# Kernel optimization log

Hardware: AMD Instinct MI355X
Metric: run time of the kernel (lower is better)

Reference implementation:

```python
import jax, jax.numpy as jnp
import numpy as np

N_NODES = 100_000
N_EDGES = 1_600_000
D_IN = 128
D_HID = 64   # hard-coded hidden width in Embedder.__init__
D_OUT = 128  # embed_dim
N_GRAPHS = 512


def setup_inputs() -> dict:
    key = jax.random.key(0)
    ks = jax.random.split(key, 10)
    x = jax.random.normal(ks[0], (N_NODES, D_IN), dtype=jnp.float32)
    edge_index = jax.random.randint(ks[1], (2, N_EDGES), 0, N_NODES, dtype=jnp.int64)
    batch_index = jnp.sort(jax.random.randint(ks[2], (N_NODES,), 0, N_GRAPHS, dtype=jnp.int64))
    def glorot(k, fan_in, fan_out):
        s = 1.0 / np.sqrt(fan_in)
        return jax.random.uniform(k, (fan_in, fan_out), jnp.float32, -s, s)
    # layer 1: SAGEConv(D_IN -> D_HID); layer 2: SAGEConv(D_HID -> D_OUT)
    return {
        "x": x,
        "W1_l": glorot(ks[3], D_IN, D_HID),   # applied to mean-aggregated neighbors
        "W1_r": glorot(ks[4], D_IN, D_HID),   # applied to root node
        "b1": jnp.zeros((D_HID,), jnp.float32),
        "W2_l": glorot(ks[5], D_HID, D_OUT),
        "W2_r": glorot(ks[6], D_HID, D_OUT),
        "b2": jnp.zeros((D_OUT,), jnp.float32),
        "edge_index": edge_index,
        "batch_index": batch_index,
    }


def _sage_conv(x, edge_index, W_l, W_r, b):
    # PyG SAGEConv with mean aggregation:
    # out_i = (mean_{j in N(i)} x_j) @ W_l + x_i @ W_r + b
    src, dst = edge_index[0], edge_index[1]
    n = x.shape[0]
    agg = jax.ops.segment_sum(x[src], dst, num_segments=n)          # [N, F]
    deg = jax.ops.segment_sum(jnp.ones((src.shape[0],), x.dtype), dst, num_segments=n)
    mean_nbr = agg / jnp.maximum(deg, 1.0)[:, None]
    return mean_nbr @ W_l + x @ W_r + b


def reference(x, W1_l, W1_r, b1, W2_l, W2_r, b2, edge_index, batch_index):
    h = _sage_conv(x, edge_index, W1_l, W1_r, b1)
    h = jax.nn.relu(h)
    h = _sage_conv(h, edge_index, W2_l, W2_r, b2)
    # F.dropout(p=0.5, training=False) -> identity in eval mode
    # gap: global mean pool per graph
    sums = jax.ops.segment_sum(h, batch_index, num_segments=N_GRAPHS)
    cnts = jax.ops.segment_sum(jnp.ones((h.shape[0],), h.dtype), batch_index, num_segments=N_GRAPHS)
    return sums / jnp.maximum(cnts, 1.0)[:, None]
```

## Files before the change

kernel.cpp:

```cpp
#include <hip/hip_runtime.h>

#define NN   100000
#define NE   1600000
#define DIN  128
#define DH   64
#define DOUT 128
#define NG   512

#define NB   391
#define EPB  6250
#define MSZ  (NB*256)

typedef short short8 __attribute__((ext_vector_type(8)));
typedef float floatx4 __attribute__((ext_vector_type(4)));

__device__ __forceinline__ unsigned short f2bf(float f) {
  unsigned b = __float_as_uint(f);
  b += 0x7FFF + ((b >> 16) & 1);
  return (unsigned short)(b >> 16);
}
__device__ __forceinline__ float bflo(unsigned u) {
  return __uint_as_float(u << 16);
}
__device__ __forceinline__ float bfhi(unsigned u) {
  return __uint_as_float(u & 0xFFFF0000u);
}
__device__ __forceinline__ unsigned pack2(float a, float b) {
  return (unsigned)f2bf(a) | ((unsigned)f2bf(b) << 16);
}

__global__ __launch_bounds__(256) void histA_kernel(
    const int* __restrict__ dst, int* __restrict__ cnt) {
  __shared__ int h[NB];
  for (int i = threadIdx.x; i < NB; i += 256) h[i] = 0;
  __syncthreads();
  int start = blockIdx.x * EPB, end = start + EPB;
  for (int e = start + threadIdx.x; e < end; e += 256)
    atomicAdd(&h[dst[e] >> 8], 1);
  __syncthreads();
  for (int b = threadIdx.x; b < NB; b += 256)
    cnt[b * 256 + blockIdx.x] = h[b];
}

__global__ __launch_bounds__(256) void reduce_kernel(
    const int* __restrict__ cnt, int* __restrict__ partials) {
  __shared__ int s[256];
  int i = blockIdx.x * 256 + threadIdx.x;
  s[threadIdx.x] = cnt[i];
  __syncthreads();
  for (int off = 128; off > 0; off >>= 1) {
    if (threadIdx.x < off) s[threadIdx.x] += s[threadIdx.x + off];
    __syncthreads();
  }
  if (threadIdx.x == 0) partials[blockIdx.x] = s[0];
}

__global__ __launch_bounds__(256) void scanpart_kernel(int* __restrict__ partials) {
  __shared__ int s[NB];
  for (int i = threadIdx.x; i < NB; i += 256) s[i] = partials[i];
  __syncthreads();
  if (threadIdx.x == 0) {
    int run = 0;
    for (int i = 0; i < NB; ++i) { int v = s[i]; s[i] = run; run += v; }
  }
  __syncthreads();
  for (int i = threadIdx.x; i < NB; i += 256) partials[i] = s[i];
}

__global__ __launch_bounds__(256) void scanfinal_kernel(
    const int* __restrict__ cnt, const int* __restrict__ partials,
    int* __restrict__ scanned) {
  __shared__ int s[256];
  int t = threadIdx.x;
  int i = blockIdx.x * 256 + t;
  int c = cnt[i];
  s[t] = c;
  __syncthreads();
  for (int off = 1; off < 256; off <<= 1) {
    int v = (t >= off) ? s[t - off] : 0;
    __syncthreads();
    s[t] += v;
    __syncthreads();
  }
  scanned[i] = s[t] - c + partials[blockIdx.x];
}

__global__ __launch_bounds__(256) void partA_kernel(
    const int* __restrict__ src, const int* __restrict__ dst,
    const int* __restrict__ scanned, int* __restrict__ part) {
  __shared__ int cur[NB];
  for (int i = threadIdx.x; i < NB; i += 256)
    cur[i] = scanned[i * 256 + blockIdx.x];
  __syncthreads();
  int start = blockIdx.x * EPB, end = start + EPB;
  for (int e = start + threadIdx.x; e < end; e += 256) {
    int d = dst[e], s = src[e];
    int pos = atomicAdd(&cur[d >> 8], 1);
    part[pos] = ((d & 255) << 17) | s;
  }
}

__global__ __launch_bounds__(256) void bucket_csr_kernel(
    const int* __restrict__ part, const int* __restrict__ scanned,
    int* __restrict__ row_start, int* __restrict__ eidx) {
  int b = blockIdx.x, t = threadIdx.x;
  int ebeg = scanned[b * 256];
  int eend = (b == NB - 1) ? NE : scanned[(b + 1) * 256];
  int nbase = b << 8;
  int nloc = NN - nbase; if (nloc > 256) nloc = 256;
  __shared__ int cntL[256];
  __shared__ int exclL[256];
  cntL[t] = 0;
  __syncthreads();
  for (int e = ebeg + t; e < eend; e += 256)
    atomicAdd(&cntL[part[e] >> 17], 1);
  __syncthreads();
  int c = cntL[t];
  exclL[t] = c;
  __syncthreads();
  for (int off = 1; off < 256; off <<= 1) {
    int v = (t >= off) ? exclL[t - off] : 0;
    __syncthreads();
    exclL[t] += v;
    __syncthreads();
  }
  int excl = exclL[t] - c;
  if (t < nloc) row_start[nbase + t] = ebeg + excl;
  if (b == NB - 1 && t == 0) row_start[NN] = NE;
  cntL[t] = excl;
  __syncthreads();
  for (int e = ebeg + t; e < eend; e += 256) {
    int v = part[e];
    int pos = atomicAdd(&cntL[v >> 17], 1);
    eidx[ebeg + pos] = v & 0x1FFFF;
  }
}

__global__ __launch_bounds__(256) void bounds_kernel(
    const int* __restrict__ batch, int* __restrict__ gs) {
  int g = blockIdx.x * 256 + threadIdx.x;
  if (g > NG) return;
  if (g == NG) { gs[NG] = NN; return; }
  int lo = 0, hi = NN;
  while (lo < hi) {
    int mid = (lo + hi) >> 1;
    if (batch[mid] < g) lo = mid + 1; else hi = mid;
  }
  gs[g] = lo;
}

__global__ __launch_bounds__(256) void split_w_kernel(
    const float* __restrict__ W1l, const float* __restrict__ W1r,
    short* __restrict__ wfrag) {
  int i = blockIdx.x * 256 + threadIdx.x;
  if (i >= DIN * DH) return;
  int k = i >> 6, n = i & 63;
  int kt = k >> 5, kin = k & 31;
  int lane = ((kin >> 3) << 4) | (n & 15);
  int j8 = kin & 7;
  int jt = n >> 4;
  float wl = W1l[i], wr = W1r[i];
  unsigned bl_ = __float_as_uint(wl);
  unsigned br_ = __float_as_uint(wr);
  short hl = (short)(bl_ >> 16);
  short hr = (short)(br_ >> 16);
  float rl = wl - __uint_as_float(bl_ & 0xFFFF0000u);
  float rr = wr - __uint_as_float(br_ & 0xFFFF0000u);
  short ll = (short)(__float_as_uint(rl) >> 16);
  short lr = (short)(__float_as_uint(rr) >> 16);
  int base0 = (((kt * 2 + 0) * 4 + jt) * 2) * 512 + lane * 8 + j8;
  int base1 = (((kt * 2 + 1) * 4 + jt) * 2) * 512 + lane * 8 + j8;
  wfrag[base0]       = hl;
  wfrag[base0 + 512] = ll;
  wfrag[base1]       = hr;
  wfrag[base1 + 512] = lr;
}

__global__ __launch_bounds__(256) void proj_mfma_kernel(
    const float* __restrict__ x, const short* __restrict__ wfrag,
    const float* __restrict__ b1, unsigned short* __restrict__ xlb,
    float* __restrict__ xr) {
  __shared__ short sB[32768];
  {
    const float4* wf4 = (const float4*)wfrag;
    float4* sB4 = (float4*)sB;
    for (int i = threadIdx.x; i < 4096; i += 256) sB4[i] = wf4[i];
  }
  __syncthreads();

  int wave = threadIdx.x >> 6;
  int lane = threadIdx.x & 63;
  int m = lane & 15, q = lane >> 4;
  int tpair = blockIdx.x * 4 + wave;
  int tile0 = tpair * 2, tile1 = tile0 + 1;
  if (tile0 >= 6250) return;

  int r0 = tile0 * 16 + m;
  int r1 = tile1 * 16 + m; if (r1 > NN - 1) r1 = NN - 1;
  const float4* xa = (const float4*)x + (size_t)r0 * 32 + q * 2;
  const float4* xb = (const float4*)x + (size_t)r1 * 32 + q * 2;

  floatx4 acc0[8], acc1[8];
#pragma unroll
  for (int a = 0; a < 8; ++a) {
    acc0[a] = (floatx4){0.f, 0.f, 0.f, 0.f};
    acc1[a] = (floatx4){0.f, 0.f, 0.f, 0.f};
  }

#pragma unroll
  for (int kt = 0; kt < 4; ++kt) {
    float4 p0 = xa[kt * 8];
    float4 p1 = xa[kt * 8 + 1];
    float4 p2 = xb[kt * 8];
    float4 p3 = xb[kt * 8 + 1];
    float af0[8] = {p0.x, p0.y, p0.z, p0.w, p1.x, p1.y, p1.z, p1.w};
    float af1[8] = {p2.x, p2.y, p2.z, p2.w, p3.x, p3.y, p3.z, p3.w};
    short8 ah0, al0, ah1, al1;
#pragma unroll
    for (int e = 0; e < 8; ++e) {
      unsigned b0 = __float_as_uint(af0[e]);
      ah0[e] = (short)(b0 >> 16);
      float lo0 = af0[e] - __uint_as_float(b0 & 0xFFFF0000u);
      al0[e] = (short)(__float_as_uint(lo0) >> 16);
      unsigned b1_ = __float_as_uint(af1[e]);
      ah1[e] = (short)(b1_ >> 16);
      float lo1 = af1[e] - __uint_as_float(b1_ & 0xFFFF0000u);
      al1[e] = (short)(__float_as_uint(lo1) >> 16);
    }
#pragma unroll
    for (int mat = 0; mat < 2; ++mat) {
#pragma unroll
      for (int jt = 0; jt < 4; ++jt) {
        int unit = ((kt * 2 + mat) * 4 + jt) * 2;
        short8 bh = *(const short8*)(sB + unit * 512 + lane * 8);
        short8 bl = *(const short8*)(sB + (unit + 1) * 512 + lane * 8);
        floatx4 c0 = acc0[mat * 4 + jt];
        c0 = __builtin_amdgcn_mfma_f32_16x16x32_bf16(ah0, bh, c0, 0, 0, 0);
        c0 = __builtin_amdgcn_mfma_f32_16x16x32_bf16(ah0, bl, c0, 0, 0, 0);
        c0 = __builtin_amdgcn_mfma_f32_16x16x32_bf16(al0, bh, c0, 0, 0, 0);
        acc0[mat * 4 + jt] = c0;
        floatx4 c1 = acc1[mat * 4 + jt];
        c1 = __builtin_amdgcn_mfma_f32_16x16x32_bf16(ah1, bh, c1, 0, 0, 0);
        c1 = __builtin_amdgcn_mfma_f32_16x16x32_bf16(ah1, bl, c1, 0, 0, 0);
        c1 = __builtin_amdgcn_mfma_f32_16x16x32_bf16(al1, bh, c1, 0, 0, 0);
        acc1[mat * 4 + jt] = c1;
      }
    }
  }

#pragma unroll
  for (int jt = 0; jt < 4; ++jt) {
    int j = jt * 16 + m;
    float bj = b1[j];
    floatx4 cl0 = acc0[jt], cr0 = acc0[4 + jt];
    floatx4 cl1 = acc1[jt], cr1 = acc1[4 + jt];
#pragma unroll
    for (int r = 0; r < 4; ++r) {
      int n0 = tile0 * 16 + q * 4 + r;
      xlb[(size_t)n0 * DH + j] = f2bf(cl0[r]);
      xr[(size_t)n0 * DH + j] = cr0[r] + bj;
    }
    if (tile1 < 6250) {
#pragma unroll
      for (int r = 0; r < 4; ++r) {
        int n1 = tile1 * 16 + q * 4 + r;
        xlb[(size_t)n1 * DH + j] = f2bf(cl1[r]);
        xr[(size_t)n1 * DH + j] = cr1[r] + bj;
      }
    }
  }
}

template <bool RELU_ADD>
__global__ __launch_bounds__(256) void gather_kernel(
    const uint2* __restrict__ feat2, const int* __restrict__ row_start,
    const int* __restrict__ eidx, const float4* __restrict__ xr4,
    uint2* __restrict__ out2) {
  int t = blockIdx.x * 256 + threadIdx.x;
  int node = t >> 4;
  if (node >= NN) return;
  int fl = t & 15;
  int rs = row_start[node], re = row_start[node + 1];
  float a0 = 0.f, a1 = 0.f, a2 = 0.f, a3 = 0.f;
  int k = rs;
  for (; k + 8 <= re; k += 8) {
    uint2 v[8];
#pragma unroll
    for (int u = 0; u < 8; ++u) v[u] = feat2[(size_t)eidx[k + u] * 16 + fl];
#pragma unroll
    for (int u = 0; u < 8; ++u) {
      a0 += bflo(v[u].x); a1 += bfhi(v[u].x);
      a2 += bflo(v[u].y); a3 += bfhi(v[u].y);
    }
  }
  for (; k + 2 <= re; k += 2) {
    uint2 v0 = feat2[(size_t)eidx[k] * 16 + fl];
    uint2 v1 = feat2[(size_t)eidx[k + 1] * 16 + fl];
    a0 += bflo(v0.x) + bflo(v1.x); a1 += bfhi(v0.x) + bfhi(v1.x);
    a2 += bflo(v0.y) + bflo(v1.y); a3 += bfhi(v0.y) + bfhi(v1.y);
  }
  if (k < re) {
    uint2 v = feat2[(size_t)eidx[k] * 16 + fl];
    a0 += bflo(v.x); a1 += bfhi(v.x);
    a2 += bflo(v.y); a3 += bfhi(v.y);
  }
  float inv = 1.0f / fmaxf((float)(re - rs), 1.0f);
  a0 *= inv; a1 *= inv; a2 *= inv; a3 *= inv;
  if (RELU_ADD) {
    float4 r = xr4[(size_t)node * 16 + fl];
    a0 = fmaxf(a0 + r.x, 0.f); a1 = fmaxf(a1 + r.y, 0.f);
    a2 = fmaxf(a2 + r.z, 0.f); a3 = fmaxf(a3 + r.w, 0.f);
  }
  uint2 o;
  o.x = pack2(a0, a1);
  o.y = pack2(a2, a3);
  out2[(size_t)node * 16 + fl] = o;
}

__global__ __launch_bounds__(256) void pool_kernel(
    const unsigned short* __restrict__ hb, const unsigned short* __restrict__ mb,
    const int* __restrict__ gs, float* __restrict__ hs,
    float* __restrict__ ms) {
  int g = blockIdx.x;
  int start = gs[g], end = gs[g + 1];
  int slot = threadIdx.x >> 6, j = threadIdx.x & 63;
  float sh = 0.f, sm = 0.f;
  for (int n = start + slot; n < end; n += 4) {
    sh += bflo((unsigned)hb[(size_t)n * DH + j]);
    sm += bflo((unsigned)mb[(size_t)n * DH + j]);
  }
  __shared__ float red[2][4][DH];
  red[0][slot][j] = sh;
  red[1][slot][j] = sm;
  __syncthreads();
  if (slot == 0) {
    sh = red[0][0][j] + red[0][1][j] + red[0][2][j] + red[0][3][j];
    sm = red[1][0][j] + red[1][1][j] + red[1][2][j] + red[1][3][j];
    hs[g * DH + j] = sh;
    ms[g * DH + j] = sm;
  }
}

__global__ __launch_bounds__(128) void final_kernel(
    const float* __restrict__ hs, const float* __restrict__ ms,
    const float* __restrict__ W2l, const float* __restrict__ W2r,
    const float* __restrict__ b2, const int* __restrict__ gs,
    float* __restrict__ out) {
  int g = blockIdx.x;
  int j = threadIdx.x;
  float n = (float)(gs[g + 1] - gs[g]);
  float acc = 0.f;
#pragma unroll 8
  for (int k = 0; k < DH; ++k)
    acc += ms[g * DH + k] * W2l[k * DOUT + j] + hs[g * DH + k] * W2r[k * DOUT + j];
  float inv = 1.0f / fmaxf(n, 1.0f);
  out[g * DOUT + j] = (acc + n * b2[j]) * inv;
}

extern "C" void kernel_launch(void* const* d_in, const int* in_sizes, int n_in,
                              void* d_out, int out_size, void* d_ws, size_t ws_size,
                              hipStream_t stream) {
  (void)in_sizes; (void)n_in; (void)out_size; (void)ws_size;
  const float* x   = (const float*)d_in[0];
  const float* W1l = (const float*)d_in[1];
  const float* W1r = (const float*)d_in[2];
  const float* b1  = (const float*)d_in[3];
  const float* W2l = (const float*)d_in[4];
  const float* W2r = (const float*)d_in[5];
  const float* b2  = (const float*)d_in[6];
  const int*   ei  = (const int*)d_in[7];
  const int*   batch = (const int*)d_in[8];
  const int* src = ei;
  const int* dst = ei + NE;
  float* out = (float*)d_out;

  char* ws = (char*)d_ws;
  unsigned short* xlb = (unsigned short*)(ws);
  unsigned short* hb  = (unsigned short*)(ws + 12800000);
  unsigned short* mb  = (unsigned short*)(ws + 25600000);
  int*  part      = (int*)(ws + 51200000);
  int*  cnt       = (int*)(ws + 57600000);
  int*  scanned   = (int*)(ws + 58000384);
  float* xr       = (float*)(ws + 51200000);
  int*  eidx      = (int*)(ws + 76800000);
  int*  row_start = (int*)(ws + 83200000);
  int*   gs       = (int*)(ws + 83600128);
  float* hs       = (float*)(ws + 83604224);
  float* msum     = (float*)(ws + 83735296);
  short* wfrag    = (short*)(ws + 83900032);
  int*  partials  = (int*)(ws + 84400128);

  const int gBlocks = (NN * 16) / 256;
  const int pBlocks = 782;

  split_w_kernel<<<32, 256, 0, stream>>>(W1l, W1r, wfrag);
  histA_kernel<<<256, 256, 0, stream>>>(dst, cnt);
  reduce_kernel<<<NB, 256, 0, stream>>>(cnt, partials);
  scanpart_kernel<<<1, 256, 0, stream>>>(partials);
  scanfinal_kernel<<<NB, 256, 0, stream>>>(cnt, partials, scanned);
  partA_kernel<<<256, 256, 0, stream>>>(src, dst, scanned, part);
  bucket_csr_kernel<<<NB, 256, 0, stream>>>(part, scanned, row_start, eidx);
  bounds_kernel<<<3, 256, 0, stream>>>(batch, gs);

  proj_mfma_kernel<<<pBlocks, 256, 0, stream>>>(x, wfrag, b1, xlb, xr);
  gather_kernel<true><<<gBlocks, 256, 0, stream>>>(
      (const uint2*)xlb, row_start, eidx, (const float4*)xr, (uint2*)hb);

  gather_kernel<false><<<gBlocks, 256, 0, stream>>>(
      (const uint2*)hb, row_start, eidx, nullptr, (uint2*)mb);

  pool_kernel<<<NG, 256, 0, stream>>>(hb, mb, gs, hs, msum);
  final_kernel<<<NG, 128, 0, stream>>>(hs, msum, W2l, W2r, b2, gs, out);
}
```

Measured before the change: 266.2 us.

## Widen gather loads to 16 bytes, store root projection in bf16, fuse pool and final

```diff
diff --git a/kernel.cpp b/kernel.cpp
--- a/kernel.cpp
+++ b/kernel.cpp
@@ -179,7 +179,7 @@
 __global__ __launch_bounds__(256) void proj_mfma_kernel(
     const float* __restrict__ x, const short* __restrict__ wfrag,
     const float* __restrict__ b1, unsigned short* __restrict__ xlb,
-    float* __restrict__ xr) {
+    unsigned short* __restrict__ xrb) {
   __shared__ short sB[32768];
   {
     const float4* wf4 = (const float4*)wfrag;
@@ -258,14 +258,14 @@
     for (int r = 0; r < 4; ++r) {
       int n0 = tile0 * 16 + q * 4 + r;
       xlb[(size_t)n0 * DH + j] = f2bf(cl0[r]);
-      xr[(size_t)n0 * DH + j] = cr0[r] + bj;
+      xrb[(size_t)n0 * DH + j] = f2bf(cr0[r] + bj);
     }
     if (tile1 < 6250) {
 #pragma unroll
       for (int r = 0; r < 4; ++r) {
         int n1 = tile1 * 16 + q * 4 + r;
         xlb[(size_t)n1 * DH + j] = f2bf(cl1[r]);
-        xr[(size_t)n1 * DH + j] = cr1[r] + bj;
+        xrb[(size_t)n1 * DH + j] = f2bf(cr1[r] + bj);
       }
     }
   }
@@ -273,88 +273,100 @@
 
 template <bool RELU_ADD>
 __global__ __launch_bounds__(256) void gather_kernel(
-    const uint2* __restrict__ feat2, const int* __restrict__ row_start,
-    const int* __restrict__ eidx, const float4* __restrict__ xr4,
-    uint2* __restrict__ out2) {
+    const uint4* __restrict__ feat4, const int* __restrict__ row_start,
+    const int* __restrict__ eidx, const uint4* __restrict__ xr4,
+    uint4* __restrict__ out4) {
   int t = blockIdx.x * 256 + threadIdx.x;
-  int node = t >> 4;
+  int node = t >> 3;
   if (node >= NN) return;
-  int fl = t & 15;
+  int fl = t & 7;
   int rs = row_start[node], re = row_start[node + 1];
   float a0 = 0.f, a1 = 0.f, a2 = 0.f, a3 = 0.f;
+  float a4 = 0.f, a5 = 0.f, a6 = 0.f, a7 = 0.f;
   int k = rs;
   for (; k + 8 <= re; k += 8) {
-    uint2 v[8];
-#pragma unroll
-    for (int u = 0; u < 8; ++u) v[u] = feat2[(size_t)eidx[k + u] * 16 + fl];
+    uint4 v[8];
+#pragma unroll
+    for (int u = 0; u < 8; ++u) v[u] = feat4[(size_t)eidx[k + u] * 8 + fl];
 #pragma unroll
     for (int u = 0; u < 8; ++u) {
       a0 += bflo(v[u].x); a1 += bfhi(v[u].x);
       a2 += bflo(v[u].y); a3 += bfhi(v[u].y);
+      a4 += bflo(v[u].z); a5 += bfhi(v[u].z);
+      a6 += bflo(v[u].w); a7 += bfhi(v[u].w);
     }
   }
   for (; k + 2 <= re; k += 2) {
-    uint2 v0 = feat2[(size_t)eidx[k] * 16 + fl];
-    uint2 v1 = feat2[(size_t)eidx[k + 1] * 16 + fl];
+    uint4 v0 = feat4[(size_t)eidx[k] * 8 + fl];
+    uint4 v1 = feat4[(size_t)eidx[k + 1] * 8 + fl];
     a0 += bflo(v0.x) + bflo(v1.x); a1 += bfhi(v0.x) + bfhi(v1.x);
     a2 += bflo(v0.y) + bflo(v1.y); a3 += bfhi(v0.y) + bfhi(v1.y);
+    a4 += bflo(v0.z) + bflo(v1.z); a5 += bfhi(v0.z) + bfhi(v1.z);
+    a6 += bflo(v0.w) + bflo(v1.w); a7 += bfhi(v0.w) + bfhi(v1.w);
   }
   if (k < re) {
-    uint2 v = feat2[(size_t)eidx[k] * 16 + fl];
+    uint4 v = feat4[(size_t)eidx[k] * 8 + fl];
     a0 += bflo(v.x); a1 += bfhi(v.x);
     a2 += bflo(v.y); a3 += bfhi(v.y);
+    a4 += bflo(v.z); a5 += bfhi(v.z);
+    a6 += bflo(v.w); a7 += bfhi(v.w);
   }
   float inv = 1.0f / fmaxf((float)(re - rs), 1.0f);
   a0 *= inv; a1 *= inv; a2 *= inv; a3 *= inv;
+  a4 *= inv; a5 *= inv; a6 *= inv; a7 *= inv;
   if (RELU_ADD) {
-    float4 r = xr4[(size_t)node * 16 + fl];
-    a0 = fmaxf(a0 + r.x, 0.f); a1 = fmaxf(a1 + r.y, 0.f);
-    a2 = fmaxf(a2 + r.z, 0.f); a3 = fmaxf(a3 + r.w, 0.f);
-  }
-  uint2 o;
+    uint4 r = xr4[(size_t)node * 8 + fl];
+    a0 = fmaxf(a0 + bflo(r.x), 0.f); a1 = fmaxf(a1 + bfhi(r.x), 0.f);
+    a2 = fmaxf(a2 + bflo(r.y), 0.f); a3 = fmaxf(a3 + bfhi(r.y), 0.f);
+    a4 = fmaxf(a4 + bflo(r.z), 0.f); a5 = fmaxf(a5 + bfhi(r.z), 0.f);
+    a6 = fmaxf(a6 + bflo(r.w), 0.f); a7 = fmaxf(a7 + bfhi(r.w), 0.f);
+  }
+  uint4 o;
   o.x = pack2(a0, a1);
   o.y = pack2(a2, a3);
-  out2[(size_t)node * 16 + fl] = o;
-}
-
-__global__ __launch_bounds__(256) void pool_kernel(
-    const unsigned short* __restrict__ hb, const unsigned short* __restrict__ mb,
-    const int* __restrict__ gs, float* __restrict__ hs,
-    float* __restrict__ ms) {
+  o.z = pack2(a4, a5);
+  o.w = pack2(a6, a7);
+  out4[(size_t)node * 8 + fl] = o;
+}
+
+__global__ __launch_bounds__(256) void pool_final_kernel(
+    const unsigned* __restrict__ hb2, const unsigned* __restrict__ mb2,
+    const int* __restrict__ gs, const float* __restrict__ W2l,
+    const float* __restrict__ W2r, const float* __restrict__ b2,
+    float* __restrict__ out) {
   int g = blockIdx.x;
   int start = gs[g], end = gs[g + 1];
-  int slot = threadIdx.x >> 6, j = threadIdx.x & 63;
-  float sh = 0.f, sm = 0.f;
-  for (int n = start + slot; n < end; n += 4) {
-    sh += bflo((unsigned)hb[(size_t)n * DH + j]);
-    sm += bflo((unsigned)mb[(size_t)n * DH + j]);
-  }
-  __shared__ float red[2][4][DH];
-  red[0][slot][j] = sh;
-  red[1][slot][j] = sm;
-  __syncthreads();
-  if (slot == 0) {
-    sh = red[0][0][j] + red[0][1][j] + red[0][2][j] + red[0][3][j];
-    sm = red[1][0][j] + red[1][1][j] + red[1][2][j] + red[1][3][j];
-    hs[g * DH + j] = sh;
-    ms[g * DH + j] = sm;
-  }
-}
-
-__global__ __launch_bounds__(128) void final_kernel(
-    const float* __restrict__ hs, const float* __restrict__ ms,
-    const float* __restrict__ W2l, const float* __restrict__ W2r,
-    const float* __restrict__ b2, const int* __restrict__ gs,
-    float* __restrict__ out) {
-  int g = blockIdx.x;
+  int slot = threadIdx.x >> 5;
+  int j2   = threadIdx.x & 31;
+  float sh0 = 0.f, sh1 = 0.f, sm0 = 0.f, sm1 = 0.f;
+  for (int n = start + slot; n < end; n += 8) {
+    unsigned hv = hb2[(size_t)n * 32 + j2];
+    unsigned mv = mb2[(size_t)n * 32 + j2];
+    sh0 += bflo(hv); sh1 += bfhi(hv);
+    sm0 += bflo(mv); sm1 += bfhi(mv);
+  }
+  __shared__ float redh[8][DH];
+  __shared__ float redm[8][DH];
+  redh[slot][j2 * 2] = sh0; redh[slot][j2 * 2 + 1] = sh1;
+  redm[slot][j2 * 2] = sm0; redm[slot][j2 * 2 + 1] = sm1;
+  __syncthreads();
+  __shared__ float hsL[DH], msL[DH];
+  if (threadIdx.x < DH) {
+    float a = 0.f, b = 0.f;
+#pragma unroll
+    for (int s = 0; s < 8; ++s) { a += redh[s][threadIdx.x]; b += redm[s][threadIdx.x]; }
+    hsL[threadIdx.x] = a; msL[threadIdx.x] = b;
+  }
+  __syncthreads();
   int j = threadIdx.x;
-  float n = (float)(gs[g + 1] - gs[g]);
-  float acc = 0.f;
+  if (j < DOUT) {
+    float n = (float)(end - start);
+    float acc = 0.f;
 #pragma unroll 8
-  for (int k = 0; k < DH; ++k)
-    acc += ms[g * DH + k] * W2l[k * DOUT + j] + hs[g * DH + k] * W2r[k * DOUT + j];
-  float inv = 1.0f / fmaxf(n, 1.0f);
-  out[g * DOUT + j] = (acc + n * b2[j]) * inv;
+    for (int k = 0; k < DH; ++k)
+      acc += msL[k] * W2l[k * DOUT + j] + hsL[k] * W2r[k * DOUT + j];
+    out[g * DOUT + j] = (acc + n * b2[j]) / fmaxf(n, 1.0f);
+  }
 }
 
 extern "C" void kernel_launch(void* const* d_in, const int* in_sizes, int n_in,
@@ -378,19 +390,17 @@
   unsigned short* xlb = (unsigned short*)(ws);
   unsigned short* hb  = (unsigned short*)(ws + 12800000);
   unsigned short* mb  = (unsigned short*)(ws + 25600000);
+  unsigned short* xrb = (unsigned short*)(ws + 38400000);
   int*  part      = (int*)(ws + 51200000);
   int*  cnt       = (int*)(ws + 57600000);
   int*  scanned   = (int*)(ws + 58000384);
-  float* xr       = (float*)(ws + 51200000);
   int*  eidx      = (int*)(ws + 76800000);
   int*  row_start = (int*)(ws + 83200000);
   int*   gs       = (int*)(ws + 83600128);
-  float* hs       = (float*)(ws + 83604224);
-  float* msum     = (float*)(ws + 83735296);
   short* wfrag    = (short*)(ws + 83900032);
   int*  partials  = (int*)(ws + 84400128);
 
-  const int gBlocks = (NN * 16) / 256;
+  const int gBlocks = (NN * 8 + 255) / 256;
   const int pBlocks = 782;
 
   split_w_kernel<<<32, 256, 0, stream>>>(W1l, W1r, wfrag);
@@ -402,13 +412,13 @@
   bucket_csr_kernel<<<NB, 256, 0, stream>>>(part, scanned, row_start, eidx);
   bounds_kernel<<<3, 256, 0, stream>>>(batch, gs);
 
-  proj_mfma_kernel<<<pBlocks, 256, 0, stream>>>(x, wfrag, b1, xlb, xr);
+  proj_mfma_kernel<<<pBlocks, 256, 0, stream>>>(x, wfrag, b1, xlb, xrb);
   gather_kernel<true><<<gBlocks, 256, 0, stream>>>(
-      (const uint2*)xlb, row_start, eidx, (const float4*)xr, (uint2*)hb);
+      (const uint4*)xlb, row_start, eidx, (const uint4*)xrb, (uint4*)hb);
 
   gather_kernel<false><<<gBlocks, 256, 0, stream>>>(
-      (const uint2*)hb, row_start, eidx, nullptr, (uint2*)mb);
-
-  pool_kernel<<<NG, 256, 0, stream>>>(hb, mb, gs, hs, msum);
-  final_kernel<<<NG, 128, 0, stream>>>(hs, msum, W2l, W2r, b2, gs, out);
-}
+      (const uint4*)hb, row_start, eidx, nullptr, (uint4*)mb);
+
+  pool_final_kernel<<<NG, 256, 0, stream>>>(
+      (const unsigned*)hb, (const unsigned*)mb, gs, W2l, W2r, b2, out);
+}
```

Measured after the change: 252.8 us. 5.1% less time.
